# Kernel tuning notes

Measured on AMD Instinct MI355X. Metric: run time of the kernel, lower is better.

## Reference

```python
import jax, jax.numpy as jnp
import numpy as np

B, S, D_IN, D_OUT = 4, 4096, 1024, 64

def setup_inputs() -> dict:
    key = jax.random.key(0)
    ks = jax.random.split(key, 7)
    return {
        "x":  jax.random.normal(ks[0], (B, S, D_IN), dtype=jnp.float32),
        "Wq": jax.random.normal(ks[1], (D_IN, D_OUT), dtype=jnp.float32) * 0.02,
        "bq": jax.random.normal(ks[2], (D_OUT,), dtype=jnp.float32) * 0.02,
        "Wk": jax.random.normal(ks[3], (D_IN, D_OUT), dtype=jnp.float32) * 0.02,
        "bk": jax.random.normal(ks[4], (D_OUT,), dtype=jnp.float32) * 0.02,
        "Wv": jax.random.normal(ks[5], (D_IN, D_OUT), dtype=jnp.float32) * 0.02,
        "bv": jax.random.normal(ks[6], (D_OUT,), dtype=jnp.float32) * 0.02,
    }

def reference(x, Wq, bq, Wk, bk, Wv, bv):
    # x: [B, S, d_in]
    seq = x.shape[1]
    q = x @ Wq + bq            # [B, S, d_out]
    k = x @ Wk + bk
    v = x @ Wv + bv
    scores = jnp.einsum("bqd,bkd->bqk", q, k)          # [B, S, S]
    causal = jnp.triu(jnp.ones((seq, seq), dtype=bool), k=1)
    scores = jnp.where(causal[None, :, :], -jnp.inf, scores)
    # NOTE: original code scales by sqrt(token_len), not sqrt(d_out) (d_k = keys.shape[1])
    scale = jnp.sqrt(jnp.asarray(seq, dtype=scores.dtype))
    attn = jax.nn.softmax(scores / scale, axis=-1)      # [B, S, S]
    # dropout in the original is applied but its result is discarded -> no-op
    return jnp.einsum("bqk,bkd->bqd", attn, v)          # [B, S, d_out]
```

## Files before the change

kernel.cpp:

```cpp
#include <hip/hip_runtime.h>
#include <math.h>

#define B 4
#define S 4096
#define DIN 1024
#define DOUT 64
#define BS (B * S)

typedef __bf16 bf16;
typedef __bf16 bf16x4 __attribute__((ext_vector_type(4)));
typedef __bf16 bf16x8 __attribute__((ext_vector_type(8)));
typedef float f32x4 __attribute__((ext_vector_type(4)));

#define QSCALE 0.022542110013890053f

#define QS_OFF 0
#define KF_OFF (2u * 1024 * 1024)
#define VF_OFF (4u * 1024 * 1024)
#define WP_OFF (6u * 1024 * 1024)
#define OP_OFF (7u * 1024 * 1024)
#define LP_OFF (23u * 1024 * 1024)

__global__ __launch_bounds__(256) void wpack_kernel(
    const float* __restrict__ Wq, const float* __restrict__ Wk,
    const float* __restrict__ Wv, bf16* __restrict__ wp) {
  const int t = blockIdx.x * 256 + threadIdx.x;
  const int m = t >> 16;
  const int r = t & 65535;
  const int k = r >> 6;
  const int n64 = r & 63;
  const float* W = (m == 0) ? Wq : (m == 1) ? Wk : Wv;
  const float v = W[r];
  const int n = m * 64 + n64;
  const int nt = n >> 4;
  const int lane = ((k >> 3) & 3) * 16 + (n & 15);
  const int idx = ((nt * 32 + (k >> 5)) * 64 + lane) * 8 + (k & 7);
  wp[idx] = (bf16)v;
}

__global__ __launch_bounds__(256) void qkv_mfma_kernel(
    const float* __restrict__ x, const float* __restrict__ bq,
    const float* __restrict__ bk, const float* __restrict__ bv,
    const bf16* __restrict__ wp, bf16* __restrict__ Qs,
    bf16* __restrict__ KF, bf16* __restrict__ VF) {
  __shared__ __align__(16) bf16 xt[64][520];

  const int tid = threadIdx.x;
  const int wid = tid >> 6;
  const int lane = tid & 63;
  const int l15 = lane & 15;
  const int quad = lane >> 4;
  const int blk = blockIdx.x;

  const bf16x8* wp8 = (const bf16x8*)wp;

  f32x4 acc[3][4];
#pragma unroll
  for (int j = 0; j < 3; ++j)
#pragma unroll
    for (int s = 0; s < 4; ++s) acc[j][s] = (f32x4)(0.f);

  for (int ph = 0; ph < 2; ++ph) {
    if (ph) __syncthreads();
#pragma unroll
    for (int bst = 0; bst < 4; ++bst) {
      float4 v[8];
#pragma unroll
      for (int i = 0; i < 8; ++i) {
        const int ch = (bst * 8 + i) * 256 + tid;
        v[i] = *(const float4*)(x + (size_t)(blk * 64 + (ch >> 7)) * DIN +
                                ph * 512 + (ch & 127) * 4);
      }
#pragma unroll
      for (int i = 0; i < 8; ++i) {
        const int ch = (bst * 8 + i) * 256 + tid;
        bf16x4 c4;
        c4[0] = (bf16)v[i].x; c4[1] = (bf16)v[i].y;
        c4[2] = (bf16)v[i].z; c4[3] = (bf16)v[i].w;
        *(bf16x4*)&xt[ch >> 7][(ch & 127) * 4] = c4;
      }
    }
    __syncthreads();

#pragma unroll 4
    for (int kc = 0; kc < 16; ++kc) {
      bf16x8 bfr[3];
#pragma unroll
      for (int j = 0; j < 3; ++j)
        bfr[j] = wp8[((wid * 3 + j) * 32 + ph * 16 + kc) * 64 + lane];
      bf16x8 a[4];
#pragma unroll
      for (int s = 0; s < 4; ++s)
        a[s] = *(const bf16x8*)&xt[s * 16 + l15][quad * 8 + kc * 32];
#pragma unroll
      for (int j = 0; j < 3; ++j)
#pragma unroll
        for (int s = 0; s < 4; ++s)
          acc[j][s] = __builtin_amdgcn_mfma_f32_16x16x32_bf16(
              a[s], bfr[j], acc[j][s], 0, 0, 0);
    }
  }

#pragma unroll
  for (int j = 0; j < 3; ++j) {
    const int nt = wid * 3 + j;
    const int sel = nt >> 2;
    const int c = (nt & 3) * 16 + l15;
    const float bias = ((sel == 0) ? bq : (sel == 1) ? bk : bv)[c];
#pragma unroll
    for (int s = 0; s < 4; ++s) {
      const int row0 = blk * 64 + s * 16 + quad * 4;
      if (sel == 0) {
#pragma unroll
        for (int r = 0; r < 4; ++r)
          Qs[(size_t)(row0 + r) * DOUT + c] =
              (bf16)((acc[j][s][r] + bias) * QSCALE);
      } else if (sel == 1) {
        const size_t kb =
            ((size_t)(((row0 >> 6) * 4 + ((row0 >> 4) & 3)) * 2 + (c >> 5)) * 64 +
             ((c >> 3) & 3) * 16 + quad * 4) * 8 + (c & 7);
#pragma unroll
        for (int r = 0; r < 4; ++r)
          KF[kb + r * 8] = (bf16)(acc[j][s][r] + bias);
      } else {
        const size_t vb =
            ((size_t)(((row0 >> 6) * 2 + ((row0 >> 5) & 1)) * 4 + (c >> 4)) * 64 +
             (c & 15) + 16 * ((row0 >> 3) & 3)) * 8 + (row0 & 7);
        bf16x4 vv;
#pragma unroll
        for (int r = 0; r < 4; ++r) vv[r] = (bf16)(acc[j][s][r] + bias);
        *(bf16x4*)(VF + vb) = vv;
      }
    }
  }
}

__global__ __launch_bounds__(256) void attn_mfma_kernel(
    const bf16* __restrict__ Qs, const bf16* __restrict__ KFp,
    const bf16* __restrict__ VFp, bf16* __restrict__ Oh,
    float* __restrict__ lh) {
  __shared__ __align__(16) bf16 pw[4][32][72];

  const int tid = threadIdx.x;
  const int wid = tid >> 6;
  const int lane = tid & 63;
  const int l15 = lane & 15;
  const int quad = lane >> 4;
  const int b = blockIdx.x & 3;
  const int half = (blockIdx.x >> 2) & 1;
  const int s32 = 127 - (blockIdx.x >> 3);
  const int ntiles = (s32 >> 1) + 1;
  const int e = half * 4 + wid;
  const int t0 = (e * ntiles) >> 3;
  const int t1 = ((e + 1) * ntiles) >> 3;

  const bf16x8* KF8 = (const bf16x8*)KFp;
  const bf16x8* VF8 = (const bf16x8*)VFp;
  const int tb0 = b * 64;

  const bf16* Qb = Qs + ((size_t)b * S + s32 * 32) * DOUT;
  bf16x8 qf[2][2];
#pragma unroll
  for (int st = 0; st < 2; ++st)
#pragma unroll
    for (int k = 0; k < 2; ++k)
      qf[st][k] =
          *(const bf16x8*)(Qb + (st * 16 + l15) * DOUT + k * 32 + quad * 8);

  f32x4 o[2][4];
#pragma unroll
  for (int st = 0; st < 2; ++st)
#pragma unroll
    for (int i = 0; i < 4; ++i) o[st][i] = (f32x4)(0.f);
  f32x4 lsum[2] = {(f32x4)(0.f), (f32x4)(0.f)};

  for (int t = t0; t < t1; ++t) {
    const int tb = tb0 + t;
    bf16x8 kf[8], vf[8];
#pragma unroll
    for (int nt = 0; nt < 4; ++nt)
#pragma unroll
      for (int c = 0; c < 2; ++c)
        kf[nt * 2 + c] = KF8[(size_t)((tb * 4 + nt) * 2 + c) * 64 + lane];
#pragma unroll
    for (int c = 0; c < 2; ++c)
#pragma unroll
      for (int ntd = 0; ntd < 4; ++ntd)
        vf[c * 4 + ntd] = VF8[(size_t)((tb * 2 + c) * 4 + ntd) * 64 + lane];

    f32x4 s[2][4];
#pragma unroll
    for (int st = 0; st < 2; ++st)
#pragma unroll
      for (int nt = 0; nt < 4; ++nt) {
        s[st][nt] = __builtin_amdgcn_mfma_f32_16x16x32_bf16(
            qf[st][0], kf[nt * 2 + 0], (f32x4)(0.f), 0, 0, 0);
        s[st][nt] = __builtin_amdgcn_mfma_f32_16x16x32_bf16(
            qf[st][1], kf[nt * 2 + 1], s[st][nt], 0, 0, 0);
      }

    if (t == ntiles - 1) {
#pragma unroll
      for (int st = 0; st < 2; ++st)
#pragma unroll
        for (int nt = 0; nt < 4; ++nt) {
          const int key = t * 64 + nt * 16 + l15;
#pragma unroll
          for (int r = 0; r < 4; ++r) {
            const int qrow = s32 * 32 + st * 16 + quad * 4 + r;
            const float p = (key <= qrow) ? exp2f(fminf(s[st][nt][r], 44.f)) : 0.f;
            lsum[st][r] += p;
            pw[wid][st * 16 + quad * 4 + r][nt * 16 + l15] = (bf16)p;
          }
        }
    } else {
#pragma unroll
      for (int st = 0; st < 2; ++st)
#pragma unroll
        for (int nt = 0; nt < 4; ++nt)
#pragma unroll
          for (int r = 0; r < 4; ++r) {
            const float p = exp2f(fminf(s[st][nt][r], 44.f));
            lsum[st][r] += p;
            pw[wid][st * 16 + quad * 4 + r][nt * 16 + l15] = (bf16)p;
          }
    }

#pragma unroll
    for (int st = 0; st < 2; ++st) {
      const bf16x8 pf0 = *(const bf16x8*)&pw[wid][st * 16 + l15][quad * 8];
      const bf16x8 pf1 = *(const bf16x8*)&pw[wid][st * 16 + l15][32 + quad * 8];
#pragma unroll
      for (int ntd = 0; ntd < 4; ++ntd) {
        o[st][ntd] = __builtin_amdgcn_mfma_f32_16x16x32_bf16(
            pf0, vf[0 * 4 + ntd], o[st][ntd], 0, 0, 0);
        o[st][ntd] = __builtin_amdgcn_mfma_f32_16x16x32_bf16(
            pf1, vf[1 * 4 + ntd], o[st][ntd], 0, 0, 0);
      }
    }
  }

#pragma unroll
  for (int m = 1; m < 16; m <<= 1)
#pragma unroll
    for (int st = 0; st < 2; ++st)
#pragma unroll
      for (int r = 0; r < 4; ++r) lsum[st][r] += __shfl_xor(lsum[st][r], m, 64);

  const int slot = (b * 128 + s32) * 8 + e;
  if (l15 == 0) {
#pragma unroll
    for (int st = 0; st < 2; ++st)
#pragma unroll
      for (int r = 0; r < 4; ++r)
        lh[slot * 32 + st * 16 + quad * 4 + r] = lsum[st][r];
  }
#pragma unroll
  for (int st = 0; st < 2; ++st)
#pragma unroll
    for (int ntd = 0; ntd < 4; ++ntd)
#pragma unroll
      for (int r = 0; r < 4; ++r)
        Oh[(size_t)slot * 2048 + (st * 16 + quad * 4 + r) * 64 + ntd * 16 + l15] =
            (bf16)o[st][ntd][r];
}

__global__ __launch_bounds__(256) void combine_kernel(
    const bf16* __restrict__ Oh, const float* __restrict__ lh,
    float* __restrict__ out) {
  const int gid = blockIdx.x * 256 + threadIdx.x;
  const int token = gid >> 4;
  const int d4 = (gid & 15) * 4;
  const int b = token >> 12;
  const int s = token & 4095;
  const int s32 = s >> 5;
  const int qq = s & 31;
  const int slot0 = (b * 128 + s32) * 8;
  f32x4 acc = (f32x4)(0.f);
  float l = 0.f;
#pragma unroll
  for (int q = 0; q < 8; ++q) {
    const bf16x4 ov =
        *(const bf16x4*)(Oh + (size_t)(slot0 + q) * 2048 + qq * 64 + d4);
#pragma unroll
    for (int i = 0; i < 4; ++i) acc[i] += (float)ov[i];
    l += lh[(slot0 + q) * 32 + qq];
  }
  ((f32x4*)out)[gid] = acc * (1.f / l);
}

extern "C" void kernel_launch(void* const* d_in, const int* in_sizes, int n_in,
                              void* d_out, int out_size, void* d_ws,
                              size_t ws_size, hipStream_t stream) {
  const float* x  = (const float*)d_in[0];
  const float* Wq = (const float*)d_in[1];
  const float* bq = (const float*)d_in[2];
  const float* Wk = (const float*)d_in[3];
  const float* bk = (const float*)d_in[4];
  const float* Wv = (const float*)d_in[5];
  const float* bv = (const float*)d_in[6];
  float* out = (float*)d_out;

  char* ws = (char*)d_ws;
  bf16* Qs = (bf16*)(ws + QS_OFF);
  bf16* KF = (bf16*)(ws + KF_OFF);
  bf16* VF = (bf16*)(ws + VF_OFF);
  bf16* wp = (bf16*)(ws + WP_OFF);
  bf16* Oh = (bf16*)(ws + OP_OFF);
  float* lh = (float*)(ws + LP_OFF);

  wpack_kernel<<<768, 256, 0, stream>>>(Wq, Wk, Wv, wp);
  qkv_mfma_kernel<<<256, 256, 0, stream>>>(x, bq, bk, bv, wp, Qs, KF, VF);
  attn_mfma_kernel<<<1024, 256, 0, stream>>>(Qs, KF, VF, Oh, lh);
  combine_kernel<<<1024, 256, 0, stream>>>(Oh, lh, out);
}
```

Baseline: 148.4 us.

## Fuse split-KV combine into attention kernel via last-block atomic counter

Removes the separate combine kernel launch. Each of the two half-blocks handling a 32-query tile increments a per-tile counter after writing its partial output and row sums. The second arrival reads all 8 partials and writes the normalized result. The counters are zeroed in the weight-pack kernel. This saves a launch and the tail gap between kernels, at the cost of a fence, an atomic, and a serialized reduction inside the attention blocks.

Measured after the change: 311.1 us. 110% more time.

```diff
diff --git a/kernel.cpp b/kernel.cpp
--- a/kernel.cpp
+++ b/kernel.cpp
@@ -20,10 +20,16 @@
 #define WP_OFF (6u * 1024 * 1024)
 #define OP_OFF (7u * 1024 * 1024)
 #define LP_OFF (23u * 1024 * 1024)
+#define CNT_OFF (30u * 1024 * 1024)
 
 __global__ __launch_bounds__(256) void wpack_kernel(
     const float* __restrict__ Wq, const float* __restrict__ Wk,
-    const float* __restrict__ Wv, bf16* __restrict__ wp) {
+    const float* __restrict__ Wv, bf16* __restrict__ wp,
+    int* __restrict__ cnt) {
+  if (blockIdx.x == 0) {
+    cnt[threadIdx.x] = 0;
+    cnt[threadIdx.x + 256] = 0;
+  }
   const int t = blockIdx.x * 256 + threadIdx.x;
   const int m = t >> 16;
   const int r = t & 65535;
@@ -138,8 +144,10 @@
 __global__ __launch_bounds__(256) void attn_mfma_kernel(
     const bf16* __restrict__ Qs, const bf16* __restrict__ KFp,
     const bf16* __restrict__ VFp, bf16* __restrict__ Oh,
-    float* __restrict__ lh) {
+    float* __restrict__ lh, int* __restrict__ cnt,
+    float* __restrict__ out) {
   __shared__ __align__(16) bf16 pw[4][32][72];
+  __shared__ int s_old;
 
   const int tid = threadIdx.x;
   const int wid = tid >> 6;
@@ -263,30 +271,34 @@
       for (int r = 0; r < 4; ++r)
         Oh[(size_t)slot * 2048 + (st * 16 + quad * 4 + r) * 64 + ntd * 16 + l15] =
             (bf16)o[st][ntd][r];
-}
-
-__global__ __launch_bounds__(256) void combine_kernel(
-    const bf16* __restrict__ Oh, const float* __restrict__ lh,
-    float* __restrict__ out) {
-  const int gid = blockIdx.x * 256 + threadIdx.x;
-  const int token = gid >> 4;
-  const int d4 = (gid & 15) * 4;
-  const int b = token >> 12;
-  const int s = token & 4095;
-  const int s32 = s >> 5;
-  const int qq = s & 31;
-  const int slot0 = (b * 128 + s32) * 8;
-  f32x4 acc = (f32x4)(0.f);
-  float l = 0.f;
-#pragma unroll
-  for (int q = 0; q < 8; ++q) {
-    const bf16x4 ov =
-        *(const bf16x4*)(Oh + (size_t)(slot0 + q) * 2048 + qq * 64 + d4);
-#pragma unroll
-    for (int i = 0; i < 4; ++i) acc[i] += (float)ov[i];
-    l += lh[(slot0 + q) * 32 + qq];
-  }
-  ((f32x4*)out)[gid] = acc * (1.f / l);
+
+  __threadfence();
+  __syncthreads();
+  if (tid == 0)
+    s_old = __hip_atomic_fetch_add(&cnt[b * 128 + s32], 1, __ATOMIC_ACQ_REL,
+                                   __HIP_MEMORY_SCOPE_AGENT);
+  __syncthreads();
+  if (s_old == 1) {
+    const int slot0 = (b * 128 + s32) * 8;
+#pragma unroll
+    for (int i = 0; i < 2; ++i) {
+      const int it = i * 256 + tid;
+      const int qq = it >> 4;
+      const int d4 = (it & 15) * 4;
+      f32x4 acc = (f32x4)(0.f);
+      float l = 0.f;
+#pragma unroll
+      for (int q = 0; q < 8; ++q) {
+        const bf16x4 ov =
+            *(const bf16x4*)(Oh + (size_t)(slot0 + q) * 2048 + qq * 64 + d4);
+#pragma unroll
+        for (int ii = 0; ii < 4; ++ii) acc[ii] += (float)ov[ii];
+        l += lh[(slot0 + q) * 32 + qq];
+      }
+      const int token = b * S + s32 * 32 + qq;
+      ((f32x4*)out)[token * 16 + (it & 15)] = acc * (1.f / l);
+    }
+  }
 }
 
 extern "C" void kernel_launch(void* const* d_in, const int* in_sizes, int n_in,
@@ -308,9 +320,9 @@
   bf16* wp = (bf16*)(ws + WP_OFF);
   bf16* Oh = (bf16*)(ws + OP_OFF);
   float* lh = (float*)(ws + LP_OFF);
-
-  wpack_kernel<<<768, 256, 0, stream>>>(Wq, Wk, Wv, wp);
+  int* cnt = (int*)(ws + CNT_OFF);
+
+  wpack_kernel<<<768, 256, 0, stream>>>(Wq, Wk, Wv, wp, cnt);
   qkv_mfma_kernel<<<256, 256, 0, stream>>>(x, bq, bk, bv, wp, Qs, KF, VF);
-  attn_mfma_kernel<<<1024, 256, 0, stream>>>(Qs, KF, VF, Oh, lh);
-  combine_kernel<<<1024, 256, 0, stream>>>(Oh, lh, out);
+  attn_mfma_kernel<<<1024, 256, 0, stream>>>(Qs, KF, VF, Oh, lh, cnt, out);
 }
```
